# Kernel optimization log

Hardware: AMD Instinct MI355X
Metric: run time of the kernel (lower is better)

The kernel has to match this reference:

```python
import jax, jax.numpy as jnp
import numpy as np

B, S, H = 2, 2048, 2304
NH, HD, NKV = 8, 256, 4
WINDOW = 512
CAP = 50.0
THETA = 10000.0
NEG_INF = -2.3819763e38


def setup_inputs() -> dict:
    key = jax.random.key(0)
    ks = jax.random.split(key, 6)
    hidden_states = jax.random.normal(ks[0], (B, S, H), dtype=jnp.float32)
    # causal additive mask (0 where attend, -inf-ish where masked)
    i = jnp.arange(S)
    causal = i[None, :] <= i[:, None]
    attention_mask = jnp.broadcast_to(
        jnp.where(causal, 0.0, NEG_INF).astype(jnp.float32)[None, None], (B, 1, S, S)
    )
    position_ids = jnp.broadcast_to(jnp.arange(S, dtype=jnp.int32)[None], (B, S))
    scale = 0.02
    Wq = jax.random.normal(ks[1], (H, NH * HD), dtype=jnp.float32) * scale
    Wk = jax.random.normal(ks[2], (H, NKV * HD), dtype=jnp.float32) * scale
    Wv = jax.random.normal(ks[3], (H, NKV * HD), dtype=jnp.float32) * scale
    Wo = jax.random.normal(ks[4], (NH * HD, H), dtype=jnp.float32) * scale
    return {
        "hidden_states": hidden_states,
        "attention_mask": attention_mask,
        "position_ids": position_ids,
        "Wq": Wq,
        "Wk": Wk,
        "Wv": Wv,
        "Wo": Wo,
    }


def _rotate_half(x):
    h = x.shape[-1] // 2
    return jnp.concatenate([-x[..., h:], x[..., :h]], axis=-1)


def reference(hidden_states, attention_mask, position_ids, Wq, Wk, Wv, Wo):
    b, s, _ = hidden_states.shape
    q = (hidden_states @ Wq).reshape(b, s, NH, HD).transpose(0, 2, 1, 3)   # [B,NH,S,HD]
    k = (hidden_states @ Wk).reshape(b, s, NKV, HD).transpose(0, 2, 1, 3)  # [B,NKV,S,HD]
    v = (hidden_states @ Wv).reshape(b, s, NKV, HD).transpose(0, 2, 1, 3)
    # rotary embedding
    inv_freq = 1.0 / (THETA ** (jnp.arange(0, HD, 2, dtype=jnp.float32) / HD))
    freqs = position_ids.astype(jnp.float32)[..., None] * inv_freq  # [B,S,HD/2]
    emb = jnp.concatenate([freqs, freqs], axis=-1)                  # [B,S,HD]
    cos = jnp.cos(emb)[:, None]  # unsqueeze head dim
    sin = jnp.sin(emb)[:, None]
    q = q * cos + _rotate_half(q) * sin
    k = k * cos + _rotate_half(k) * sin
    # GQA: repeat kv heads
    rep = NH // NKV
    k = jnp.repeat(k, rep, axis=1)
    v = jnp.repeat(v, rep, axis=1)
    logits = jnp.einsum("bhqd,bhkd->bhqk", q, k) / jnp.sqrt(jnp.float32(HD))
    # sliding-window mask: keep |i-j| <= WINDOW-1, else NEG_INF
    idx = jnp.arange(s)
    sliding = jnp.abs(idx[:, None] - idx[None, :]) <= (WINDOW - 1)
    mask = jnp.where(sliding[None, None], attention_mask, NEG_INF)
    # tanh logit softcapping, then additive mask
    logits = jnp.tanh(logits / CAP) * CAP + mask
    probs = jax.nn.softmax(logits.astype(jnp.float32), axis=-1).astype(q.dtype)
    out = jnp.einsum("bhqk,bhkd->bhqd", probs, v)
    out = out.transpose(0, 2, 1, 3).reshape(b, s, NH * HD)
    return out @ Wo
```

## Files before the change

kernel.cpp:

```cpp
#include <hip/hip_runtime.h>
#include <cmath>

#define B_   2
#define S_   2048
#define H_   2304
#define NH_  8
#define HD_  256
#define NKV_ 4
#define WIN_ 512
#define QKVW 4096

typedef unsigned short ushort_t;
typedef __attribute__((ext_vector_type(8))) short bf16x8;
typedef __attribute__((ext_vector_type(4))) float floatx4;

__device__ __forceinline__ unsigned short f2bf(float f) {
  unsigned u = __builtin_bit_cast(unsigned, f);
  u += 0x7fff + ((u >> 16) & 1);
  return (unsigned short)(u >> 16);
}
__device__ __forceinline__ float bf2f(ushort_t v) {
  unsigned u = (unsigned)v << 16;
  return __builtin_bit_cast(float, u);
}

__device__ __forceinline__ void gl2lds16(const void* g, void* l) {
  __builtin_amdgcn_global_load_lds(
      (const __attribute__((address_space(1))) unsigned int*)g,
      (__attribute__((address_space(3))) unsigned int*)l, 16, 0, 0);
}

__global__ void cast_bf16(const float* __restrict__ in, ushort_t* __restrict__ out) {
  const int i = blockIdx.x * 256 + threadIdx.x;
  float4 v = ((const float4*)in)[i];
  ushort4 o;
  o.x = f2bf(v.x); o.y = f2bf(v.y); o.z = f2bf(v.z); o.w = f2bf(v.w);
  ((ushort4*)out)[i] = o;
}

__global__ void transpose_cast(const float* __restrict__ W, ushort_t* __restrict__ Wt,
                               int K, int N) {
  __shared__ float t[32][33];
  const int lx = threadIdx.x & 31, ly = threadIdx.x >> 5;
  const int n0 = blockIdx.x * 32, k0 = blockIdx.y * 32;
#pragma unroll
  for (int i = 0; i < 4; ++i)
    t[ly + i * 8][lx] = W[(long long)(k0 + ly + i * 8) * N + n0 + lx];
  __syncthreads();
#pragma unroll
  for (int i = 0; i < 4; ++i)
    Wt[(long long)(n0 + ly + i * 8) * K + k0 + lx] = f2bf(t[lx][ly + i * 8]);
}

template <bool OUT_BF16>
__launch_bounds__(256)
__global__ void gemm_bt(const ushort_t* __restrict__ A,
                        const ushort_t* __restrict__ Bt,
                        void* __restrict__ Cv, int M, int N, int K) {
  __shared__ ushort_t As[128 * 32];
  __shared__ ushort_t Bs[128 * 32];
  const int tid = threadIdx.x, lane = tid & 63, wid = tid >> 6;
  const int bm = blockIdx.y * 128, bn = blockIdx.x * 128;
  const int wm = (wid >> 1) * 64, wn = (wid & 1) * 64;

  floatx4 acc[4][4] = {};

  const int r = lane >> 2, c = lane & 3;
  const int skey = (r >> 1) & 3;
  const int scol = (c ^ skey) * 8;
  const int srow = wid * 32 + r;
  const long long aBase = (long long)(bm + srow) * K + scol;
  const long long bBase = (long long)(bn + srow) * K + scol;
  ushort_t* AsW = &As[(wid * 32) * 32];
  ushort_t* BsW = &Bs[(wid * 32) * 32];

  const int l15 = lane & 15, lq = lane >> 4;
  const int fo = l15 * 32 + (lq ^ ((l15 >> 1) & 3)) * 8;

  for (int k0 = 0; k0 < K; k0 += 32) {
    __syncthreads();
    gl2lds16(A + aBase + k0,           AsW);
    gl2lds16(A + aBase + k0 + 16 * K,  AsW + 16 * 32);
    gl2lds16(Bt + bBase + k0,          BsW);
    gl2lds16(Bt + bBase + k0 + 16 * K, BsW + 16 * 32);
    __syncthreads();

    bf16x8 af[4], bfr[4];
#pragma unroll
    for (int i = 0; i < 4; ++i) {
      af[i]  = *(const bf16x8*)&As[(wm + i * 16) * 32 + fo];
      bfr[i] = *(const bf16x8*)&Bs[(wn + i * 16) * 32 + fo];
    }
#pragma unroll
    for (int i = 0; i < 4; ++i)
#pragma unroll
      for (int j = 0; j < 4; ++j)
        acc[i][j] = __builtin_amdgcn_mfma_f32_16x16x32_bf16(af[i], bfr[j], acc[i][j], 0, 0, 0);
  }

  const int r0 = lq * 4, c0 = l15;
#pragma unroll
  for (int i = 0; i < 4; ++i)
#pragma unroll
    for (int j = 0; j < 4; ++j) {
      const long long base = (long long)(bm + wm + i * 16 + r0) * N + bn + wn + j * 16 + c0;
      if (OUT_BF16) {
        ushort_t* Cp = (ushort_t*)Cv + base;
#pragma unroll
        for (int rr = 0; rr < 4; ++rr) Cp[(long long)rr * N] = f2bf(acc[i][j][rr]);
      } else {
        float* Cp = (float*)Cv + base;
#pragma unroll
        for (int rr = 0; rr < 4; ++rr) Cp[(long long)rr * N] = acc[i][j][rr];
      }
    }
}

__global__ void rope_inplace(ushort_t* __restrict__ QKV16, const int* __restrict__ pos) {
  const int bs  = blockIdx.x;
  const int gid = blockIdx.y * 256 + threadIdx.x;
  const int head = gid >> 7;
  const int d    = gid & 127;
  const float pp   = (float)pos[bs];
  const float invf = __expf(-(float)d * (9.210340371976184f / 128.0f));
  const float ang  = pp * invf;
  const float cc = cosf(ang), sn = sinf(ang);
  ushort_t* base = QKV16 + (size_t)bs * QKVW + head * HD_;
  const float x1 = bf2f(base[d]);
  const float x2 = bf2f(base[d + 128]);
  float o1 = x1 * cc - x2 * sn;
  float o2 = x2 * cc + x1 * sn;
  if (head < NH_) { o1 *= 0.0625f; o2 *= 0.0625f; }
  base[d]       = f2bf(o1);
  base[d + 128] = f2bf(o2);
}

__global__ void v_prep(const ushort_t* __restrict__ QKV16, ushort_t* __restrict__ Vt16) {
  __shared__ ushort_t tile[32][33];
  const int k0 = blockIdx.x * 32, d0 = blockIdx.y * 32;
  const int b = blockIdx.z >> 2, hk = blockIdx.z & 3;
  const int lx = threadIdx.x & 31, ly = threadIdx.x >> 5;
#pragma unroll
  for (int i = 0; i < 4; ++i)
    tile[ly + 8 * i][lx] =
        QKV16[(size_t)(b * S_ + k0 + ly + 8 * i) * QKVW + 3072 + hk * HD_ + d0 + lx];
  __syncthreads();
#pragma unroll
  for (int i = 0; i < 4; ++i)
    Vt16[((size_t)(b * NKV_ + hk) * HD_ + d0 + ly + 8 * i) * S_ + k0 + lx] =
        tile[lx][ly + 8 * i];
}

__launch_bounds__(256, 2)
__global__ void attn_mfma(const ushort_t* __restrict__ QKV16,
                          const ushort_t* __restrict__ Vt16,
                          ushort_t* __restrict__ AOb) {
  __shared__ ushort_t Ks[32 * 256];
  __shared__ ushort_t Vts[256 * 32];
  __shared__ ushort_t Ps[4][16 * 32];
  __shared__ float rsb[4][16];

  const int lane = threadIdx.x & 63, w = threadIdx.x >> 6;
  const int l15 = lane & 15, lq = lane >> 4;
  const int qb = blockIdx.x * 64;
  const int h = blockIdx.y, b = blockIdx.z;
  const int hk = h >> 1;

  const ushort_t* Qh = QKV16 + (size_t)b * S_ * QKVW + h * HD_;
  const ushort_t* Kh = QKV16 + (size_t)b * S_ * QKVW + 2048 + hk * HD_;
  const ushort_t* Vh = Vt16 + ((size_t)(b * NKV_ + hk) * HD_) * S_;

  const int qw = qb + w * 16;

  bf16x8 afq[8];
  {
    const ushort_t* qr = Qh + (size_t)(qw + l15) * QKVW + lq * 8;
#pragma unroll
    for (int kd = 0; kd < 8; ++kd) afq[kd] = *(const bf16x8*)(qr + kd * 32);
  }

  floatx4 acc[16] = {};
  float rs[4] = {0.f, 0.f, 0.f, 0.f};

  int kb0 = qb - (WIN_ - 1);
  if (kb0 < 0) kb0 = 0;
  kb0 &= ~31;

  const int ksp = lane & 31, ksr = lane >> 5;
  const int vsp = lane & 3,  vsr = lane >> 2;

  for (int kb = kb0; kb < qb + 64; kb += 32) {
    __syncthreads();
#pragma unroll
    for (int i = 0; i < 4; ++i) {
      const int kl = w * 8 + 2 * i + ksr;
      gl2lds16(Kh + (size_t)(kb + kl) * QKVW + (ksp ^ (kl & 31)) * 8,
               &Ks[(w * 8 + 2 * i) * 256]);
    }
#pragma unroll
    for (int i = 0; i < 4; ++i) {
      const int dl = w * 64 + 16 * i + vsr;
      gl2lds16(Vh + (size_t)dl * S_ + kb + (vsp ^ ((dl >> 1) & 3)) * 8,
               &Vts[(w * 64 + 16 * i) * 32]);
    }
    __syncthreads();

    if (kb <= qw + 15 && kb + 31 >= qw - (WIN_ - 1)) {
      ushort_t* Pw = Ps[w];
#pragma unroll
      for (int kt = 0; kt < 2; ++kt) {
        floatx4 sacc = {};
        const int keyl = kt * 16 + l15;
        const int krow = keyl * 256;
        const int ksw = keyl & 31;
#pragma unroll
        for (int kd = 0; kd < 8; ++kd) {
          bf16x8 bk = *(const bf16x8*)&Ks[krow + ((kd * 4 + lq) ^ ksw) * 8];
          sacc = __builtin_amdgcn_mfma_f32_16x16x32_bf16(afq[kd], bk, sacc, 0, 0, 0);
        }
        const int keyg = kb + keyl;
#pragma unroll
        for (int r = 0; r < 4; ++r) {
          const int qg = qw + lq * 4 + r;
          const float t = __expf(sacc[r] * 0.04f);
          const float L = 50.f - __fdividef(100.f, t + 1.f);
          float p = __expf(L);
          p = (keyg <= qg && keyg >= qg - (WIN_ - 1)) ? p : 0.f;
          rs[r] += p;
          const int ql = lq * 4 + r;
          const int ch = kt * 2 + (l15 >> 3);
          Pw[ql * 32 + ((ch ^ ((ql >> 1) & 3)) * 8) + (l15 & 7)] = f2bf(p);
        }
      }
      asm volatile("s_waitcnt lgkmcnt(0)" ::: "memory");

      const bf16x8 bp = *(const bf16x8*)&Pw[l15 * 32 + ((lq ^ ((l15 >> 1) & 3)) * 8)];
      const int vsw = (l15 >> 1) & 3;
#pragma unroll
      for (int t = 0; t < 16; ++t) {
        bf16x8 av = *(const bf16x8*)&Vts[(t * 16 + l15) * 32 + ((lq ^ vsw) * 8)];
        acc[t] = __builtin_amdgcn_mfma_f32_16x16x32_bf16(av, bp, acc[t], 0, 0, 0);
      }
    }
  }

#pragma unroll
  for (int r = 0; r < 4; ++r) {
    rs[r] += __shfl_xor(rs[r], 1, 64);
    rs[r] += __shfl_xor(rs[r], 2, 64);
    rs[r] += __shfl_xor(rs[r], 4, 64);
    rs[r] += __shfl_xor(rs[r], 8, 64);
  }
  if (l15 == 0) {
#pragma unroll
    for (int r = 0; r < 4; ++r) rsb[w][lq * 4 + r] = rs[r];
  }
  asm volatile("s_waitcnt lgkmcnt(0)" ::: "memory");
  __builtin_amdgcn_wave_barrier();
  const float inv = 1.0f / rsb[w][l15];

  const size_t ob = ((size_t)(b * S_ + qw + l15) * NH_ + h) * HD_;
#pragma unroll
  for (int t = 0; t < 16; ++t) {
    ushort4 o;
    o.x = f2bf(acc[t][0] * inv);
    o.y = f2bf(acc[t][1] * inv);
    o.z = f2bf(acc[t][2] * inv);
    o.w = f2bf(acc[t][3] * inv);
    *(ushort4*)&AOb[ob + t * 16 + lq * 4] = o;
  }
}

extern "C" void kernel_launch(void* const* d_in, const int* in_sizes, int n_in,
                              void* d_out, int out_size, void* d_ws, size_t ws_size,
                              hipStream_t stream) {
  const float* X   = (const float*)d_in[0];
  const int*   pos = (const int*)d_in[2];
  const float* Wq  = (const float*)d_in[3];
  const float* Wk  = (const float*)d_in[4];
  const float* Wv  = (const float*)d_in[5];
  const float* Wo  = (const float*)d_in[6];
  float* out = (float*)d_out;

  const int M  = B_ * S_;
  const int NQ = NH_ * HD_;
  const int NK = NKV_ * HD_;

  char* w = (char*)d_ws;
  ushort_t* QKV16 = (ushort_t*)w;  w += (size_t)M * QKVW * 2;
  ushort_t* Xb    = (ushort_t*)w;  w += (size_t)M * H_ * 2;
  ushort_t* Wqkvt = (ushort_t*)w;  w += (size_t)QKVW * H_ * 2;
  ushort_t* Wot   = (ushort_t*)w;  w += (size_t)H_ * NQ * 2;
  ushort_t* Vt16  = (ushort_t*)w;  w += (size_t)B_ * NKV_ * S_ * HD_ * 2;
  ushort_t* AOb   = (ushort_t*)w;  w += (size_t)M * NQ * 2;

  dim3 blk(256);

  cast_bf16<<<(M * H_) / 1024, blk, 0, stream>>>(X, Xb);
  transpose_cast<<<dim3(NQ / 32, H_ / 32), blk, 0, stream>>>(Wq, Wqkvt, H_, NQ);
  transpose_cast<<<dim3(NK / 32, H_ / 32), blk, 0, stream>>>(Wk, Wqkvt + (size_t)2048 * H_, H_, NK);
  transpose_cast<<<dim3(NK / 32, H_ / 32), blk, 0, stream>>>(Wv, Wqkvt + (size_t)3072 * H_, H_, NK);
  transpose_cast<<<dim3(H_ / 32, NQ / 32), blk, 0, stream>>>(Wo, Wot, NQ, H_);

  gemm_bt<true><<<dim3(QKVW / 128, M / 128), blk, 0, stream>>>(Xb, Wqkvt, QKV16, M, QKVW, H_);

  rope_inplace<<<dim3(M, 6), blk, 0, stream>>>(QKV16, pos);
  v_prep<<<dim3(S_ / 32, HD_ / 32, B_ * NKV_), blk, 0, stream>>>(QKV16, Vt16);

  attn_mfma<<<dim3(S_ / 64, NH_, B_), blk, 0, stream>>>(QKV16, Vt16, AOb);

  gemm_bt<false><<<dim3(H_ / 128, M / 128), blk, 0, stream>>>(AOb, Wot, out, M, H_, NQ);
}
```

Before: 420.1 us.

## Use 32x32 MFMA in GEMM and share KV tiles across GQA head pairs

The GEMM inner loop switches from 16x16x32 MFMA tiles to 32x32x16 MFMA tiles. Each wave now holds a 2x2 grid of 16-element accumulators, which halves the LDS fragment loads per MFMA. The attention kernel now launches 512-thread blocks that cover both query heads sharing one KV head. Each K/V tile loaded into LDS is reused by two heads, halving KV global traffic and the number of blocks. In exchange, the GEMM epilogue writes to scattered rows, and the larger attention blocks may cut occupancy and raise barrier cost.

Result: faster. 406.4 us (-3.2%).

```diff
diff --git a/kernel.cpp b/kernel.cpp
--- a/kernel.cpp
+++ b/kernel.cpp
@@ -13,6 +13,7 @@
 typedef unsigned short ushort_t;
 typedef __attribute__((ext_vector_type(8))) short bf16x8;
 typedef __attribute__((ext_vector_type(4))) float floatx4;
+typedef __attribute__((ext_vector_type(16))) float floatx16;
 
 __device__ __forceinline__ unsigned short f2bf(float f) {
   unsigned u = __builtin_bit_cast(unsigned, f);
@@ -63,7 +64,7 @@
   const int bm = blockIdx.y * 128, bn = blockIdx.x * 128;
   const int wm = (wid >> 1) * 64, wn = (wid & 1) * 64;
 
-  floatx4 acc[4][4] = {};
+  floatx16 acc[2][2] = {};
 
   const int r = lane >> 2, c = lane & 3;
   const int skey = (r >> 1) & 3;
@@ -74,8 +75,8 @@
   ushort_t* AsW = &As[(wid * 32) * 32];
   ushort_t* BsW = &Bs[(wid * 32) * 32];
 
-  const int l15 = lane & 15, lq = lane >> 4;
-  const int fo = l15 * 32 + (lq ^ ((l15 >> 1) & 3)) * 8;
+  const int l31 = lane & 31, lg = lane >> 5;
+  const int swz = (l31 >> 1) & 3;
 
   for (int k0 = 0; k0 < K; k0 += 32) {
     __syncthreads();
@@ -85,34 +86,38 @@
     gl2lds16(Bt + bBase + k0 + 16 * K, BsW + 16 * 32);
     __syncthreads();
 
-    bf16x8 af[4], bfr[4];
-#pragma unroll
-    for (int i = 0; i < 4; ++i) {
-      af[i]  = *(const bf16x8*)&As[(wm + i * 16) * 32 + fo];
-      bfr[i] = *(const bf16x8*)&Bs[(wn + i * 16) * 32 + fo];
-    }
-#pragma unroll
-    for (int i = 0; i < 4; ++i)
-#pragma unroll
-      for (int j = 0; j < 4; ++j)
-        acc[i][j] = __builtin_amdgcn_mfma_f32_16x16x32_bf16(af[i], bfr[j], acc[i][j], 0, 0, 0);
-  }
-
-  const int r0 = lq * 4, c0 = l15;
-#pragma unroll
-  for (int i = 0; i < 4; ++i)
-#pragma unroll
-    for (int j = 0; j < 4; ++j) {
-      const long long base = (long long)(bm + wm + i * 16 + r0) * N + bn + wn + j * 16 + c0;
-      if (OUT_BF16) {
-        ushort_t* Cp = (ushort_t*)Cv + base;
-#pragma unroll
-        for (int rr = 0; rr < 4; ++rr) Cp[(long long)rr * N] = f2bf(acc[i][j][rr]);
-      } else {
-        float* Cp = (float*)Cv + base;
-#pragma unroll
-        for (int rr = 0; rr < 4; ++rr) Cp[(long long)rr * N] = acc[i][j][rr];
+    bf16x8 af[2][2], bfr[2][2];
+#pragma unroll
+    for (int mt = 0; mt < 2; ++mt)
+#pragma unroll
+      for (int h = 0; h < 2; ++h) {
+        af[mt][h]  = *(const bf16x8*)&As[(wm + 32 * mt + l31) * 32 + ((2 * h + lg) ^ swz) * 8];
+        bfr[mt][h] = *(const bf16x8*)&Bs[(wn + 32 * mt + l31) * 32 + ((2 * h + lg) ^ swz) * 8];
       }
+#pragma unroll
+    for (int h = 0; h < 2; ++h)
+#pragma unroll
+      for (int mt = 0; mt < 2; ++mt)
+#pragma unroll
+        for (int nt = 0; nt < 2; ++nt)
+          acc[mt][nt] = __builtin_amdgcn_mfma_f32_32x32x16_bf16(af[mt][h], bfr[nt][h],
+                                                                acc[mt][nt], 0, 0, 0);
+  }
+
+#pragma unroll
+  for (int mt = 0; mt < 2; ++mt)
+#pragma unroll
+    for (int nt = 0; nt < 2; ++nt) {
+      const int col = bn + wn + 32 * nt + l31;
+#pragma unroll
+      for (int g = 0; g < 4; ++g)
+#pragma unroll
+        for (int rr = 0; rr < 4; ++rr) {
+          const int row = bm + wm + 32 * mt + rr + 8 * g + 4 * lg;
+          const float v = acc[mt][nt][g * 4 + rr];
+          if (OUT_BF16) ((ushort_t*)Cv)[(long long)row * N + col] = f2bf(v);
+          else          ((float*)Cv)[(long long)row * N + col]    = v;
+        }
     }
 }
 
@@ -151,26 +156,27 @@
         tile[lx][ly + 8 * i];
 }
 
-__launch_bounds__(256, 2)
+__launch_bounds__(512)
 __global__ void attn_mfma(const ushort_t* __restrict__ QKV16,
                           const ushort_t* __restrict__ Vt16,
                           ushort_t* __restrict__ AOb) {
   __shared__ ushort_t Ks[32 * 256];
   __shared__ ushort_t Vts[256 * 32];
-  __shared__ ushort_t Ps[4][16 * 32];
-  __shared__ float rsb[4][16];
+  __shared__ ushort_t Ps[8][16 * 32];
+  __shared__ float rsb[8][16];
 
   const int lane = threadIdx.x & 63, w = threadIdx.x >> 6;
   const int l15 = lane & 15, lq = lane >> 4;
   const int qb = blockIdx.x * 64;
-  const int h = blockIdx.y, b = blockIdx.z;
-  const int hk = h >> 1;
+  const int hp = blockIdx.y, b = blockIdx.z;
+  const int h  = hp * 2 + (w >> 2);
+  const int hw = w & 3;
 
   const ushort_t* Qh = QKV16 + (size_t)b * S_ * QKVW + h * HD_;
-  const ushort_t* Kh = QKV16 + (size_t)b * S_ * QKVW + 2048 + hk * HD_;
-  const ushort_t* Vh = Vt16 + ((size_t)(b * NKV_ + hk) * HD_) * S_;
-
-  const int qw = qb + w * 16;
+  const ushort_t* Kh = QKV16 + (size_t)b * S_ * QKVW + 2048 + hp * HD_;
+  const ushort_t* Vh = Vt16 + ((size_t)(b * NKV_ + hp) * HD_) * S_;
+
+  const int qw = qb + hw * 16;
 
   bf16x8 afq[8];
   {
@@ -192,16 +198,16 @@
   for (int kb = kb0; kb < qb + 64; kb += 32) {
     __syncthreads();
 #pragma unroll
-    for (int i = 0; i < 4; ++i) {
-      const int kl = w * 8 + 2 * i + ksr;
+    for (int i = 0; i < 2; ++i) {
+      const int kl = w * 4 + 2 * i + ksr;
       gl2lds16(Kh + (size_t)(kb + kl) * QKVW + (ksp ^ (kl & 31)) * 8,
-               &Ks[(w * 8 + 2 * i) * 256]);
+               &Ks[(w * 4 + 2 * i) * 256]);
     }
 #pragma unroll
-    for (int i = 0; i < 4; ++i) {
-      const int dl = w * 64 + 16 * i + vsr;
+    for (int i = 0; i < 2; ++i) {
+      const int dl = w * 32 + 16 * i + vsr;
       gl2lds16(Vh + (size_t)dl * S_ + kb + (vsp ^ ((dl >> 1) & 3)) * 8,
-               &Vts[(w * 64 + 16 * i) * 32]);
+               &Vts[(w * 32 + 16 * i) * 32]);
     }
     __syncthreads();
 
@@ -220,14 +226,14 @@
         }
         const int keyg = kb + keyl;
 #pragma unroll
-        for (int r = 0; r < 4; ++r) {
-          const int qg = qw + lq * 4 + r;
-          const float t = __expf(sacc[r] * 0.04f);
+        for (int rr = 0; rr < 4; ++rr) {
+          const int qg = qw + lq * 4 + rr;
+          const float t = __expf(sacc[rr] * 0.04f);
           const float L = 50.f - __fdividef(100.f, t + 1.f);
           float p = __expf(L);
           p = (keyg <= qg && keyg >= qg - (WIN_ - 1)) ? p : 0.f;
-          rs[r] += p;
-          const int ql = lq * 4 + r;
+          rs[rr] += p;
+          const int ql = lq * 4 + rr;
           const int ch = kt * 2 + (l15 >> 3);
           Pw[ql * 32 + ((ch ^ ((ql >> 1) & 3)) * 8) + (l15 & 7)] = f2bf(p);
         }
@@ -245,15 +251,15 @@
   }
 
 #pragma unroll
-  for (int r = 0; r < 4; ++r) {
-    rs[r] += __shfl_xor(rs[r], 1, 64);
-    rs[r] += __shfl_xor(rs[r], 2, 64);
-    rs[r] += __shfl_xor(rs[r], 4, 64);
-    rs[r] += __shfl_xor(rs[r], 8, 64);
+  for (int rr = 0; rr < 4; ++rr) {
+    rs[rr] += __shfl_xor(rs[rr], 1, 64);
+    rs[rr] += __shfl_xor(rs[rr], 2, 64);
+    rs[rr] += __shfl_xor(rs[rr], 4, 64);
+    rs[rr] += __shfl_xor(rs[rr], 8, 64);
   }
   if (l15 == 0) {
 #pragma unroll
-    for (int r = 0; r < 4; ++r) rsb[w][lq * 4 + r] = rs[r];
+    for (int rr = 0; rr < 4; ++rr) rsb[w][lq * 4 + rr] = rs[rr];
   }
   asm volatile("s_waitcnt lgkmcnt(0)" ::: "memory");
   __builtin_amdgcn_wave_barrier();
@@ -307,7 +313,7 @@
   rope_inplace<<<dim3(M, 6), blk, 0, stream>>>(QKV16, pos);
   v_prep<<<dim3(S_ / 32, HD_ / 32, B_ * NKV_), blk, 0, stream>>>(QKV16, Vt16);
 
-  attn_mfma<<<dim3(S_ / 64, NH_, B_), blk, 0, stream>>>(QKV16, Vt16, AOb);
+  attn_mfma<<<dim3(S_ / 64, NKV_, B_), dim3(512), 0, stream>>>(QKV16, Vt16, AOb);
 
   gemm_bt<false><<<dim3(H_ / 128, M / 128), blk, 0, stream>>>(AOb, Wot, out, M, H_, NQ);
 }
```
